# Optimization experiments

Measured on AMD Instinct MI355X. Metric: run time of the kernel, lower is better.

## Reference

```python
import jax, jax.numpy as jnp
import numpy as np

B, S, D, H, E, K = 16, 2048, 768, 3072, 8, 2
CAP_FACTOR = 1.25
LN_EPS = 1e-5


def setup_inputs() -> dict:
    key = jax.random.key(0)
    ks = jax.random.split(key, 6)
    scale = 0.02
    return {
        "x": jax.random.normal(ks[0], (B, S, D), jnp.float32),
        "w_gate": jax.random.normal(ks[1], (D, E), jnp.float32) * scale,  # router (eval: no noise)
        "w1": jax.random.normal(ks[2], (E, D, H), jnp.float32) * scale,
        "b1": jnp.zeros((E, H), jnp.float32),
        "w2": jax.random.normal(ks[3], (E, H, D), jnp.float32) * scale,
        "b2": jnp.zeros((E, D), jnp.float32),
        "ln_w": jnp.ones((D,), jnp.float32),
        "ln_b": jnp.zeros((D,), jnp.float32),
    }


def reference(x, w_gate, w1, b1, w2, b2, ln_w, ln_b):
    b, s, d = x.shape
    n = b * s
    capacity = int(CAP_FACTOR * n * K / E)  # static, matches _compute_capacity
    xf = x.reshape(n, d)

    # NoisyTopKRouter in eval mode: linear gate -> top-k -> softmax over top-k logits
    logits = xf @ w_gate                                   # [N, E]
    top_logits, top_idx = jax.lax.top_k(logits, K)         # [N, K]
    routing = jax.nn.softmax(top_logits, axis=-1)          # [N, K]

    out = jnp.zeros((n, d), x.dtype)
    for e in range(E):
        # per-token weight for expert e (0 if not routed to e)
        w_e = jnp.sum(routing * (top_idx == e), axis=-1)   # [N]
        # capacity dropping: keep the `capacity` highest-weight tokens.
        # Unassigned tokens have weight 0 -> zero contribution, so selecting
        # them as filler is mathematically identical to the torch loop.
        top_w, tok = jax.lax.top_k(w_e, capacity)          # [cap], [cap]
        sel = xf[tok]                                      # gather [cap, D]
        h = jax.nn.gelu(sel @ w1[e] + b1[e], approximate=False)
        y = h @ w2[e] + b2[e]                              # [cap, D]
        out = out.at[tok].add(y * top_w[:, None])          # weighted scatter-add

    out = out.reshape(b, s, d)
    mu = jnp.mean(out, axis=-1, keepdims=True)
    var = jnp.mean(jnp.square(out - mu), axis=-1, keepdims=True)
    return (out - mu) * jax.lax.rsqrt(var + LN_EPS) * ln_w + ln_b
```

## Files before the change

### kernel.cpp

```cpp
#include <hip/hip_runtime.h>
#include <math.h>

#define NTOK 32768
#define DDIM 768
#define HDIM 3072
#define NEXP 8
#define CAP  10240

typedef short short8 __attribute__((ext_vector_type(8)));
typedef float f32x4 __attribute__((ext_vector_type(4)));

__device__ __forceinline__ unsigned short f2bf(float f) {
  unsigned u = __float_as_uint(f);
  u += 0x7FFFu + ((u >> 16) & 1u);
  return (unsigned short)(u >> 16);
}
__device__ __forceinline__ float bf2f(unsigned short h) {
  return __uint_as_float((unsigned)h << 16);
}

__device__ __forceinline__ void gload16(const void* g, void* l) {
  __builtin_amdgcn_global_load_lds(
      (const __attribute__((address_space(1))) void*)g,
      (__attribute__((address_space(3))) void*)l, 16, 0, 0);
}

__global__ __launch_bounds__(256) void router_assign(
    const float* __restrict__ x, const float* __restrict__ wg,
    unsigned short* __restrict__ xb,
    unsigned int* __restrict__ pair, float* __restrict__ pw)
{
  __shared__ float wt[NEXP][DDIM];
  int t = threadIdx.x;
  for (int idx = t; idx < NEXP * DDIM; idx += 256) {
    int d = idx >> 3, e = idx & 7;
    wt[e][d] = wg[idx];
  }
  __syncthreads();
  int wave = t >> 6, lane = t & 63;
  int n0 = blockIdx.x * 32 + wave * 8;
  for (int i = 0; i < 8; ++i) {
    int n = n0 + i;
    const float* xr = x + (size_t)n * DDIM;
    unsigned short* xbr = xb + (size_t)n * DDIM;
    float acc[NEXP];
#pragma unroll
    for (int e = 0; e < NEXP; ++e) acc[e] = 0.f;
#pragma unroll
    for (int c = 0; c < 3; ++c) {
      int d = c * 256 + lane * 4;
      float4 xv = *(const float4*)(xr + d);
      ushort4 pk;
      pk.x = f2bf(xv.x); pk.y = f2bf(xv.y); pk.z = f2bf(xv.z); pk.w = f2bf(xv.w);
      *(ushort4*)(xbr + d) = pk;
#pragma unroll
      for (int e = 0; e < NEXP; ++e) {
        float4 wv = *(const float4*)(&wt[e][d]);
        acc[e] += xv.x * wv.x + xv.y * wv.y + xv.z * wv.z + xv.w * wv.w;
      }
    }
#pragma unroll
    for (int e = 0; e < NEXP; ++e) {
      float v = acc[e];
      for (int o = 32; o > 0; o >>= 1) v += __shfl_xor(v, o, 64);
      acc[e] = v;
    }
    if (lane == 0) {
      int e1 = 0; float l1 = acc[0];
#pragma unroll
      for (int e = 1; e < NEXP; ++e) if (acc[e] > l1) { l1 = acc[e]; e1 = e; }
      int e2 = -1; float l2 = -INFINITY;
#pragma unroll
      for (int e = 0; e < NEXP; ++e) if (e != e1 && acc[e] > l2) { l2 = acc[e]; e2 = e; }
      float p1 = 1.f / (1.f + expf(l2 - l1));
      pair[n] = (unsigned)e1 | ((unsigned)e2 << 8);
      pw[n] = p1;
    }
  }
}

__global__ __launch_bounds__(256) void router_scatter(
    const unsigned int* __restrict__ pair, int* __restrict__ cnt,
    int* __restrict__ tokidx, int* __restrict__ slotof)
{
  int e = blockIdx.x;
  __shared__ int wsum[4];
  __shared__ int basev;
  int t = threadIdx.x, wave = t >> 6, lane = t & 63;
  if (t == 0) basev = 0;
  __syncthreads();
  for (int nb = 0; nb < NTOK; nb += 256) {
    int n = nb + t;
    unsigned p = pair[n];
    int e1 = p & 255, e2 = (p >> 8) & 255;
    bool m2 = (e2 == e);
    bool m = (e1 == e) | m2;
    unsigned long long bal = __ballot(m);
    int pre = __popcll(bal & ((1ull << lane) - 1ull));
    if (lane == 0) wsum[wave] = __popcll(bal);
    __syncthreads();
    int woff = 0;
    for (int wv = 0; wv < wave; ++wv) woff += wsum[wv];
    int tot = wsum[0] + wsum[1] + wsum[2] + wsum[3];
    int pos = basev + woff + pre;
    if (m) {
      if (pos < CAP) {
        tokidx[e * CAP + pos] = n;
        slotof[2 * n + (m2 ? 1 : 0)] = e * CAP + pos;
      } else {
        slotof[2 * n + (m2 ? 1 : 0)] = -1;
      }
    }
    __syncthreads();
    if (t == 0) basev += tot;
  }
  __syncthreads();
  if (t == 0) cnt[e] = (basev < CAP) ? basev : CAP;
}

__global__ __launch_bounds__(256) void transpose_kernel(
    const float* __restrict__ src, unsigned short* __restrict__ dst, int R, int C)
{
  __shared__ float tile[64][65];
  int eb = blockIdx.z;
  const float* s = src + (size_t)eb * R * C;
  unsigned short* d = dst + (size_t)eb * R * C;
  int c0 = blockIdx.x * 64, r0 = blockIdx.y * 64;
  int tc = threadIdx.x & 63, tg = threadIdx.x >> 6;
#pragma unroll
  for (int rr = tg; rr < 64; rr += 4)
    tile[rr][tc] = s[(size_t)(r0 + rr) * C + c0 + tc];
  __syncthreads();
#pragma unroll
  for (int rr = tg; rr < 64; rr += 4)
    d[(size_t)(c0 + rr) * R + r0 + tc] = f2bf(tile[tc][rr]);
}

template<int EPI, int KK, int NN>
__global__ __launch_bounds__(256, 2) void moe_gemm(
    const unsigned short* __restrict__ A,
    const unsigned short* __restrict__ Bt,
    const float* __restrict__ bias,
    const int* __restrict__ cnt,
    const int* __restrict__ tokidx,
    unsigned short* __restrict__ Obuf,
    int mbase, int Mc)
{
  int e = blockIdx.z;
  int M = cnt[e]; if (M > CAP) M = CAP;
  int ly0 = blockIdx.y * 128;
  int gm0 = mbase + ly0;
  if (gm0 >= M) return;
  int n0 = blockIdx.x * 128;
  int t = threadIdx.x, wave = t >> 6, lane = t & 63;
  int wr = wave >> 1, wc = wave & 1;
  int lane15 = lane & 15, quad = lane >> 4;

  __shared__ __align__(16) char smem[32768];
  char* ldsA = smem;
  char* ldsB = smem + 16384;

  const unsigned short* ag[4];
  const unsigned short* bg[4];
#pragma unroll
  for (int i = 0; i < 4; ++i) {
    int li = i * 256 + t;
    int r = li >> 3;
    int c = (li & 7) ^ (r & 7);
    if (EPI == 0) {
      int gr = gm0 + r; if (gr >= M) gr = M - 1;
      int ti = tokidx[e * CAP + gr];
      ag[i] = A + (size_t)ti * KK + c * 8;
    } else {
      ag[i] = A + ((size_t)e * Mc + ly0 + r) * KK + c * 8;
    }
    bg[i] = Bt + (size_t)e * NN * KK + (size_t)(n0 + r) * KK + c * 8;
  }

  int aoff[2][4], boff[2][4];
#pragma unroll
  for (int ks = 0; ks < 2; ++ks) {
#pragma unroll
    for (int f = 0; f < 4; ++f) {
      int ar = wr * 64 + f * 16 + lane15;
      aoff[ks][f] = ar * 128 + (((ks * 4 + quad) ^ (ar & 7)) * 16);
      int br = wc * 64 + f * 16 + lane15;
      boff[ks][f] = br * 128 + (((ks * 4 + quad) ^ (br & 7)) * 16);
    }
  }

  f32x4 acc[4][4];
#pragma unroll
  for (int mi = 0; mi < 4; ++mi)
#pragma unroll
    for (int ni = 0; ni < 4; ++ni)
#pragma unroll
      for (int r = 0; r < 4; ++r) acc[mi][ni][r] = 0.f;

  char* lwA = ldsA + wave * 1024;
  char* lwB = ldsB + wave * 1024;

  for (int kt = 0; kt < KK / 64; ++kt) {
    __syncthreads();
#pragma unroll
    for (int i = 0; i < 4; ++i) {
      gload16(ag[i] + kt * 64, lwA + i * 4096);
      gload16(bg[i] + kt * 64, lwB + i * 4096);
    }
    __syncthreads();
#pragma unroll
    for (int ks = 0; ks < 2; ++ks) {
      short8 af[4], bf[4];
#pragma unroll
      for (int f = 0; f < 4; ++f) af[f] = *(const short8*)(ldsA + aoff[ks][f]);
#pragma unroll
      for (int f = 0; f < 4; ++f) bf[f] = *(const short8*)(ldsB + boff[ks][f]);
#pragma unroll
      for (int mi = 0; mi < 4; ++mi)
#pragma unroll
        for (int ni = 0; ni < 4; ++ni)
          acc[mi][ni] = __builtin_amdgcn_mfma_f32_16x16x32_bf16(
              af[mi], bf[ni], acc[mi][ni], 0, 0, 0);
    }
  }

  if (EPI == 0) {
#pragma unroll
    for (int ni = 0; ni < 4; ++ni) {
      int col = n0 + wc * 64 + ni * 16 + lane15;
      float bcol = bias[e * NN + col];
#pragma unroll
      for (int mi = 0; mi < 4; ++mi) {
        int rowb = ly0 + wr * 64 + mi * 16 + quad * 4;
#pragma unroll
        for (int r = 0; r < 4; ++r) {
          float v = acc[mi][ni][r] + bcol;
          v = 0.5f * v * (1.f + erff(v * 0.70710678118654752f));
          Obuf[((size_t)e * Mc + rowb + r) * NN + col] = f2bf(v);
        }
      }
    }
  } else {
    float bc[4];
#pragma unroll
    for (int ni = 0; ni < 4; ++ni)
      bc[ni] = bias[e * NN + n0 + wc * 64 + ni * 16 + lane15];
#pragma unroll
    for (int mi = 0; mi < 4; ++mi) {
      int gmb = gm0 + wr * 64 + mi * 16 + quad * 4;
#pragma unroll
      for (int r = 0; r < 4; ++r) {
        int gm = gmb + r;
        if (gm < M) {
          unsigned short* yrow = Obuf + ((size_t)e * CAP + gm) * NN;
#pragma unroll
          for (int ni = 0; ni < 4; ++ni) {
            int col = n0 + wc * 64 + ni * 16 + lane15;
            yrow[col] = f2bf(acc[mi][ni][r] + bc[ni]);
          }
        }
      }
    }
  }
}

__global__ __launch_bounds__(256) void combine_ln(
    const unsigned short* __restrict__ Y, const int* __restrict__ slotof,
    const float* __restrict__ pw,
    const float* __restrict__ lnw, const float* __restrict__ lnb,
    float* __restrict__ out)
{
  __shared__ float red[8];
  int n = blockIdx.x;
  int s0 = slotof[2 * n], s1 = slotof[2 * n + 1];
  float p0 = pw[n], p1 = 1.f - p0;
  const unsigned short* y0 = Y + (size_t)(s0 < 0 ? 0 : s0) * DDIM;
  const unsigned short* y1 = Y + (size_t)(s1 < 0 ? 0 : s1) * DDIM;
  if (s0 < 0) p0 = 0.f;
  if (s1 < 0) p1 = 0.f;
  int t = threadIdx.x;
  float v0 = p0 * bf2f(y0[t])       + p1 * bf2f(y1[t]);
  float v1 = p0 * bf2f(y0[t + 256]) + p1 * bf2f(y1[t + 256]);
  float v2 = p0 * bf2f(y0[t + 512]) + p1 * bf2f(y1[t + 512]);
  float s = v0 + v1 + v2;
  float ss = v0 * v0 + v1 * v1 + v2 * v2;
  for (int o = 32; o > 0; o >>= 1) { s += __shfl_xor(s, o, 64); ss += __shfl_xor(ss, o, 64); }
  int wave = t >> 6, lane = t & 63;
  if (lane == 0) { red[wave] = s; red[4 + wave] = ss; }
  __syncthreads();
  s = red[0] + red[1] + red[2] + red[3];
  ss = red[4] + red[5] + red[6] + red[7];
  float mu = s * (1.f / DDIM);
  float var = ss * (1.f / DDIM) - mu * mu;
  float rs = rsqrtf(var + 1e-5f);
  float* row = out + (size_t)n * DDIM;
  row[t]       = (v0 - mu) * rs * lnw[t]       + lnb[t];
  row[t + 256] = (v1 - mu) * rs * lnw[t + 256] + lnb[t + 256];
  row[t + 512] = (v2 - mu) * rs * lnw[t + 512] + lnb[t + 512];
}

__global__ void sentinel_kernel(float* __restrict__ out, int n) {
  int i = blockIdx.x * 256 + threadIdx.x;
  if (i < n) out[i] = 12345.0f;
}

extern "C" void kernel_launch(void* const* d_in, const int* in_sizes, int n_in,
                              void* d_out, int out_size, void* d_ws, size_t ws_size,
                              hipStream_t stream)
{
  const float* x   = (const float*)d_in[0];
  const float* wg  = (const float*)d_in[1];
  const float* w1  = (const float*)d_in[2];
  const float* b1  = (const float*)d_in[3];
  const float* w2  = (const float*)d_in[4];
  const float* b2  = (const float*)d_in[5];
  const float* lnw = (const float*)d_in[6];
  const float* lnb = (const float*)d_in[7];
  float* out = (float*)d_out;

  char* ws = (char*)d_ws;
  size_t off = 0;
  auto take = [&](size_t bytes) {
    char* p = ws + off; off += (bytes + 255) & ~(size_t)255; return p;
  };
  unsigned short* xb   = (unsigned short*)take((size_t)NTOK * DDIM * 2);
  unsigned short* w1bt = (unsigned short*)take((size_t)NEXP * DDIM * HDIM * 2);
  unsigned short* w2bt = (unsigned short*)take((size_t)NEXP * DDIM * HDIM * 2);
  int*   tokidx = (int*)take((size_t)NEXP * CAP * 4);
  unsigned int* pair = (unsigned int*)take((size_t)NTOK * 4);
  float* pw   = (float*)take((size_t)NTOK * 4);
  int*   slotof = (int*)take((size_t)NTOK * 2 * 4);
  int*   cnt  = (int*)take(256);
  unsigned short* Ybuf = (unsigned short*)take((size_t)NEXP * CAP * DDIM * 2);

  size_t avail = (ws_size > off) ? (ws_size - off) : 0;
  long long cand = (long long)(avail / ((size_t)NEXP * HDIM * 2));
  int Mc = (int)((cand / 128) * 128);
  if (Mc > CAP) Mc = CAP;
  if (Mc < 128) {
    sentinel_kernel<<<(NTOK * DDIM + 255) / 256, 256, 0, stream>>>(out, NTOK * DDIM);
    return;
  }
  unsigned short* Hbuf = (unsigned short*)take((size_t)NEXP * Mc * HDIM * 2);

  router_assign<<<NTOK / 32, 256, 0, stream>>>(x, wg, xb, pair, pw);
  transpose_kernel<<<dim3(HDIM / 64, DDIM / 64, NEXP), 256, 0, stream>>>(w1, w1bt, DDIM, HDIM);
  transpose_kernel<<<dim3(DDIM / 64, HDIM / 64, NEXP), 256, 0, stream>>>(w2, w2bt, HDIM, DDIM);
  router_scatter<<<NEXP, 256, 0, stream>>>(pair, cnt, tokidx, slotof);

  for (int mbase = 0; mbase < CAP; mbase += Mc) {
    int rows = CAP - mbase; if (rows > Mc) rows = Mc;
    int mt = rows / 128;
    moe_gemm<0, DDIM, HDIM><<<dim3(HDIM / 128, mt, NEXP), 256, 0, stream>>>(
        xb, w1bt, b1, cnt, tokidx, Hbuf, mbase, Mc);
    moe_gemm<1, HDIM, DDIM><<<dim3(DDIM / 128, mt, NEXP), 256, 0, stream>>>(
        Hbuf, w2bt, b2, cnt, tokidx, Ybuf, mbase, Mc);
  }

  combine_ln<<<NTOK, 256, 0, stream>>>(Ybuf, slotof, pw, lnw, lnb, out);
}
```

Before: 1.460 ms.

## Rewrite MoE GEMM as 256x256 tile, 8-wave, double-buffered pipelined kernel

The expert GEMM moves from 128x128 tiles with 4 waves and a single LDS buffer to 256x256 tiles with 8 waves and a 128KB double-buffered LDS. Global-to-LDS loads for the next k-step are interleaved with MFMA phases under fine-grained barriers, vmcnt waits and s_setprio. The aim is to hide memory latency and raise arithmetic intensity per block. In exchange there are far fewer blocks (e.g. 12x40x8 for GEMM1, 3x40x8 for GEMM2), which risks poor CU occupancy and wave quantization, and the 128KB LDS allocation may limit residency.

```diff
diff --git a/kernel.cpp b/kernel.cpp
--- a/kernel.cpp
+++ b/kernel.cpp
@@ -137,7 +137,7 @@
 }
 
 template<int EPI, int KK, int NN>
-__global__ __launch_bounds__(256, 2) void moe_gemm(
+__global__ __launch_bounds__(512, 2) void moe_gemm(
     const unsigned short* __restrict__ A,
     const unsigned short* __restrict__ Bt,
     const float* __restrict__ bias,
@@ -146,95 +146,151 @@
     unsigned short* __restrict__ Obuf,
     int mbase, int Mc)
 {
+  constexpr int KT = KK / 64;
+  constexpr int NI = KT / 2;
   int e = blockIdx.z;
   int M = cnt[e]; if (M > CAP) M = CAP;
-  int ly0 = blockIdx.y * 128;
+  int ly0 = blockIdx.y * 256;
   int gm0 = mbase + ly0;
   if (gm0 >= M) return;
-  int n0 = blockIdx.x * 128;
+  int n0 = blockIdx.x * 256;
   int t = threadIdx.x, wave = t >> 6, lane = t & 63;
-  int wr = wave >> 1, wc = wave & 1;
+  int wr = wave >> 2, wc = wave & 3;
   int lane15 = lane & 15, quad = lane >> 4;
 
-  __shared__ __align__(16) char smem[32768];
-  char* ldsA = smem;
-  char* ldsB = smem + 16384;
-
-  const unsigned short* ag[4];
-  const unsigned short* bg[4];
-#pragma unroll
-  for (int i = 0; i < 4; ++i) {
-    int li = i * 256 + t;
-    int r = li >> 3;
-    int c = (li & 7) ^ (r & 7);
-    if (EPI == 0) {
-      int gr = gm0 + r; if (gr >= M) gr = M - 1;
-      int ti = tokidx[e * CAP + gr];
-      ag[i] = A + (size_t)ti * KK + c * 8;
-    } else {
-      ag[i] = A + ((size_t)e * Mc + ly0 + r) * KK + c * 8;
-    }
-    bg[i] = Bt + (size_t)e * NN * KK + (size_t)(n0 + r) * KK + c * 8;
-  }
-
-  int aoff[2][4], boff[2][4];
-#pragma unroll
-  for (int ks = 0; ks < 2; ++ks) {
-#pragma unroll
-    for (int f = 0; f < 4; ++f) {
-      int ar = wr * 64 + f * 16 + lane15;
-      aoff[ks][f] = ar * 128 + (((ks * 4 + quad) ^ (ar & 7)) * 16);
-      int br = wc * 64 + f * 16 + lane15;
-      boff[ks][f] = br * 128 + (((ks * 4 + quad) ^ (br & 7)) * 16);
-    }
-  }
-
-  f32x4 acc[4][4];
-#pragma unroll
-  for (int mi = 0; mi < 4; ++mi)
-#pragma unroll
-    for (int ni = 0; ni < 4; ++ni)
-#pragma unroll
-      for (int r = 0; r < 4; ++r) acc[mi][ni][r] = 0.f;
-
-  char* lwA = ldsA + wave * 1024;
-  char* lwB = ldsB + wave * 1024;
-
-  for (int kt = 0; kt < KK / 64; ++kt) {
-    __syncthreads();
-#pragma unroll
-    for (int i = 0; i < 4; ++i) {
-      gload16(ag[i] + kt * 64, lwA + i * 4096);
-      gload16(bg[i] + kt * 64, lwB + i * 4096);
-    }
-    __syncthreads();
-#pragma unroll
-    for (int ks = 0; ks < 2; ++ks) {
-      short8 af[4], bf[4];
-#pragma unroll
-      for (int f = 0; f < 4; ++f) af[f] = *(const short8*)(ldsA + aoff[ks][f]);
-#pragma unroll
-      for (int f = 0; f < 4; ++f) bf[f] = *(const short8*)(ldsB + boff[ks][f]);
-#pragma unroll
-      for (int mi = 0; mi < 4; ++mi)
-#pragma unroll
-        for (int ni = 0; ni < 4; ++ni)
-          acc[mi][ni] = __builtin_amdgcn_mfma_f32_16x16x32_bf16(
-              af[mi], bf[ni], acc[mi][ni], 0, 0, 0);
-    }
-  }
-
+  __shared__ __align__(16) char smem[131072];
+
+  int ci0 = wave * 128 + lane;
+  int ci1 = ci0 + 64;
+  int r0 = ci0 >> 2, r1 = ci1 >> 2;
+  int c0 = (ci0 & 3) ^ ((r0 >> 1) & 3);
+  int c1 = (ci1 & 3) ^ ((r1 >> 1) & 3);
+  const unsigned short *aB0, *aB1, *bB0, *bB1;
   if (EPI == 0) {
-#pragma unroll
-    for (int ni = 0; ni < 4; ++ni) {
-      int col = n0 + wc * 64 + ni * 16 + lane15;
+    int g0 = gm0 + r0; if (g0 >= M) g0 = M - 1;
+    int g1 = gm0 + r1; if (g1 >= M) g1 = M - 1;
+    aB0 = A + (size_t)tokidx[e * CAP + g0] * KK + c0 * 8;
+    aB1 = A + (size_t)tokidx[e * CAP + g1] * KK + c1 * 8;
+  } else {
+    aB0 = A + ((size_t)e * Mc + ly0 + r0) * KK + c0 * 8;
+    aB1 = A + ((size_t)e * Mc + ly0 + r1) * KK + c1 * 8;
+  }
+  bB0 = Bt + ((size_t)e * NN + n0 + r0) * KK + c0 * 8;
+  bB1 = Bt + ((size_t)e * NN + n0 + r1) * KK + c1 * 8;
+
+#define STAGE_A(buf, kh, kt_) do { \
+    gload16(aB0 + (kt_) * 64 + (kh) * 32, smem + (buf) * 65536 + (kh) * 16384 + wave * 2048); \
+    gload16(aB1 + (kt_) * 64 + (kh) * 32, smem + (buf) * 65536 + (kh) * 16384 + wave * 2048 + 1024); \
+  } while (0)
+#define STAGE_B(buf, kh, kt_) do { \
+    gload16(bB0 + (kt_) * 64 + (kh) * 32, smem + (buf) * 65536 + 32768 + (kh) * 16384 + wave * 2048); \
+    gload16(bB1 + (kt_) * 64 + (kh) * 32, smem + (buf) * 65536 + 32768 + (kh) * 16384 + wave * 2048 + 1024); \
+  } while (0)
+
+  int aoffb[8], boffb[4];
+#pragma unroll
+  for (int m = 0; m < 8; ++m) {
+    int row = wr * 128 + m * 16 + lane15;
+    aoffb[m] = row * 64 + ((quad ^ ((row >> 1) & 3)) * 16);
+  }
+#pragma unroll
+  for (int n = 0; n < 4; ++n) {
+    int row = wc * 64 + n * 16 + lane15;
+    boffb[n] = 32768 + row * 64 + ((quad ^ ((row >> 1) & 3)) * 16);
+  }
+
+  f32x4 acc[8][4];
+#pragma unroll
+  for (int mf = 0; mf < 8; ++mf)
+#pragma unroll
+    for (int n = 0; n < 4; ++n)
+#pragma unroll
+      for (int r = 0; r < 4; ++r) acc[mf][n][r] = 0.f;
+
+  short8 af[4], bf[4];
+
+#define BAR()  __builtin_amdgcn_s_barrier()
+#define WVM4() asm volatile("s_waitcnt vmcnt(4)" ::: "memory")
+#define WVM0() asm volatile("s_waitcnt vmcnt(0)" ::: "memory")
+#define RD_B(buf, ks) do { \
+    _Pragma("unroll") \
+    for (int n = 0; n < 4; ++n) \
+      bf[n] = *(const short8*)(smem + (buf) * 65536 + (ks) * 16384 + boffb[n]); \
+  } while (0)
+#define RD_A(buf, ks, mh) do { \
+    _Pragma("unroll") \
+    for (int m = 0; m < 4; ++m) \
+      af[m] = *(const short8*)(smem + (buf) * 65536 + (ks) * 16384 + aoffb[(mh) * 4 + m]); \
+  } while (0)
+#define MM(mh) do { \
+    __builtin_amdgcn_s_setprio(1); \
+    _Pragma("unroll") \
+    for (int m = 0; m < 4; ++m) \
+      _Pragma("unroll") \
+      for (int n = 0; n < 4; ++n) \
+        acc[(mh) * 4 + m][n] = __builtin_amdgcn_mfma_f32_16x16x32_bf16( \
+            af[m], bf[n], acc[(mh) * 4 + m][n], 0, 0, 0); \
+    __builtin_amdgcn_s_setprio(0); \
+  } while (0)
+
+  STAGE_A(0, 0, 0); STAGE_B(0, 0, 0);
+  STAGE_A(0, 1, 0); STAGE_B(0, 1, 0);
+  STAGE_A(1, 0, 1); STAGE_B(1, 0, 1);
+  WVM4();
+  BAR();
+
+#pragma unroll 1
+  for (int it = 0; it < NI - 1; ++it) {
+    int kt = 2 * it;
+    RD_B(0, 0); RD_A(0, 0, 0); STAGE_A(1, 1, kt + 1);
+    BAR(); MM(0); BAR();
+    RD_A(0, 0, 1); STAGE_B(1, 1, kt + 1);
+    BAR(); MM(1); BAR();
+    RD_B(0, 1); RD_A(0, 1, 0); STAGE_A(0, 0, kt + 2);
+    BAR(); MM(0); BAR();
+    RD_A(0, 1, 1); STAGE_B(0, 0, kt + 2);
+    BAR(); MM(1); WVM4(); BAR();
+    RD_B(1, 0); RD_A(1, 0, 0); STAGE_A(0, 1, kt + 2);
+    BAR(); MM(0); BAR();
+    RD_A(1, 0, 1); STAGE_B(0, 1, kt + 2);
+    BAR(); MM(1); BAR();
+    RD_B(1, 1); RD_A(1, 1, 0); STAGE_A(1, 0, kt + 3);
+    BAR(); MM(0); BAR();
+    RD_A(1, 1, 1); STAGE_B(1, 0, kt + 3);
+    BAR(); MM(1); WVM4(); BAR();
+  }
+
+  {
+    constexpr int kt = 2 * (NI - 1);
+    RD_B(0, 0); RD_A(0, 0, 0); STAGE_A(1, 1, kt + 1);
+    BAR(); MM(0); BAR();
+    RD_A(0, 0, 1); STAGE_B(1, 1, kt + 1);
+    BAR(); MM(1); BAR();
+    RD_B(0, 1); RD_A(0, 1, 0);
+    BAR(); MM(0); BAR();
+    RD_A(0, 1, 1);
+    BAR(); MM(1); WVM0(); BAR();
+    RD_B(1, 0); RD_A(1, 0, 0);
+    BAR(); MM(0); BAR();
+    RD_A(1, 0, 1);
+    BAR(); MM(1); BAR();
+    RD_B(1, 1); RD_A(1, 1, 0);
+    BAR(); MM(0); BAR();
+    RD_A(1, 1, 1);
+    BAR(); MM(1);
+  }
+
+  if (EPI == 0) {
+#pragma unroll
+    for (int n = 0; n < 4; ++n) {
+      int col = n0 + wc * 64 + n * 16 + lane15;
       float bcol = bias[e * NN + col];
 #pragma unroll
-      for (int mi = 0; mi < 4; ++mi) {
-        int rowb = ly0 + wr * 64 + mi * 16 + quad * 4;
+      for (int mf = 0; mf < 8; ++mf) {
+        int rowb = ly0 + wr * 128 + mf * 16 + quad * 4;
 #pragma unroll
         for (int r = 0; r < 4; ++r) {
-          float v = acc[mi][ni][r] + bcol;
+          float v = acc[mf][n][r] + bcol;
           v = 0.5f * v * (1.f + erff(v * 0.70710678118654752f));
           Obuf[((size_t)e * Mc + rowb + r) * NN + col] = f2bf(v);
         }
@@ -243,25 +299,33 @@
   } else {
     float bc[4];
 #pragma unroll
-    for (int ni = 0; ni < 4; ++ni)
-      bc[ni] = bias[e * NN + n0 + wc * 64 + ni * 16 + lane15];
-#pragma unroll
-    for (int mi = 0; mi < 4; ++mi) {
-      int gmb = gm0 + wr * 64 + mi * 16 + quad * 4;
+    for (int n = 0; n < 4; ++n)
+      bc[n] = bias[e * NN + n0 + wc * 64 + n * 16 + lane15];
+#pragma unroll
+    for (int mf = 0; mf < 8; ++mf) {
+      int gmb = gm0 + wr * 128 + mf * 16 + quad * 4;
 #pragma unroll
       for (int r = 0; r < 4; ++r) {
         int gm = gmb + r;
         if (gm < M) {
           unsigned short* yrow = Obuf + ((size_t)e * CAP + gm) * NN;
 #pragma unroll
-          for (int ni = 0; ni < 4; ++ni) {
-            int col = n0 + wc * 64 + ni * 16 + lane15;
-            yrow[col] = f2bf(acc[mi][ni][r] + bc[ni]);
+          for (int n = 0; n < 4; ++n) {
+            int col = n0 + wc * 64 + n * 16 + lane15;
+            yrow[col] = f2bf(acc[mf][n][r] + bc[n]);
           }
         }
       }
     }
   }
+#undef STAGE_A
+#undef STAGE_B
+#undef BAR
+#undef WVM4
+#undef WVM0
+#undef RD_B
+#undef RD_A
+#undef MM
 }
 
 __global__ __launch_bounds__(256) void combine_ln(
@@ -335,9 +399,9 @@
 
   size_t avail = (ws_size > off) ? (ws_size - off) : 0;
   long long cand = (long long)(avail / ((size_t)NEXP * HDIM * 2));
-  int Mc = (int)((cand / 128) * 128);
+  int Mc = (int)((cand / 256) * 256);
   if (Mc > CAP) Mc = CAP;
-  if (Mc < 128) {
+  if (Mc < 256) {
     sentinel_kernel<<<(NTOK * DDIM + 255) / 256, 256, 0, stream>>>(out, NTOK * DDIM);
     return;
   }
@@ -350,10 +414,10 @@
 
   for (int mbase = 0; mbase < CAP; mbase += Mc) {
     int rows = CAP - mbase; if (rows > Mc) rows = Mc;
-    int mt = rows / 128;
-    moe_gemm<0, DDIM, HDIM><<<dim3(HDIM / 128, mt, NEXP), 256, 0, stream>>>(
+    int mt = rows / 256;
+    moe_gemm<0, DDIM, HDIM><<<dim3(HDIM / 256, mt, NEXP), 512, 0, stream>>>(
         xb, w1bt, b1, cnt, tokidx, Hbuf, mbase, Mc);
-    moe_gemm<1, HDIM, DDIM><<<dim3(DDIM / 128, mt, NEXP), 256, 0, stream>>>(
+    moe_gemm<1, HDIM, DDIM><<<dim3(DDIM / 256, mt, NEXP), 512, 0, stream>>>(
         Hbuf, w2bt, b2, cnt, tokidx, Ybuf, mbase, Mc);
   }
 
```

After: 1.558 ms. +6.7%, slower.
